# Kernel tuning notes

Measured on AMD Instinct MI355X. Metric: run time of the kernel, lower is better.

## Reference

```python
import jax, jax.numpy as jnp
import numpy as np

DIM = 768
HEADS = 12
DH = DIM // HEADS


def setup_inputs() -> dict:
    key = jax.random.key(0)
    ks = jax.random.split(key, 5)
    b, n = 2, 4096
    x = jax.random.normal(ks[0], (b, n, DIM), dtype=jnp.float32)
    # to_qkv: Linear(dim -> 3*heads*dh)
    w_qkv = jax.random.normal(ks[1], (DIM, 3 * HEADS * DH), dtype=jnp.float32) * (DIM ** -0.5)
    b_qkv = jax.random.normal(ks[2], (3 * HEADS * DH,), dtype=jnp.float32) * 0.01
    # out: Linear(heads*dh -> dim)
    w_out = jax.random.normal(ks[3], (HEADS * DH, DIM), dtype=jnp.float32) * ((HEADS * DH) ** -0.5)
    b_out = jax.random.normal(ks[4], (DIM,), dtype=jnp.float32) * 0.01
    return {"x": x, "w_qkv": w_qkv, "b_qkv": b_qkv, "w_out": w_out, "b_out": b_out}


def reference(x, w_qkv, b_qkv, w_out, b_out):
    b, n, _ = x.shape
    scale = DIM ** -0.5  # NOTE: module scales by dim**-0.5, not d_h**-0.5
    qkv = x @ w_qkv + b_qkv                        # [b, n, 3*h*d]
    q, k, v = jnp.split(qkv, 3, axis=-1)
    def to_heads(t):
        return t.reshape(b, n, HEADS, DH).transpose(0, 2, 1, 3)  # [b, h, n, d]
    q, k, v = to_heads(q), to_heads(k), to_heads(v)
    dots = jnp.einsum('bhid,bhjd->bhij', q, k) * scale  # [b, h, n, n]
    attn = jax.nn.softmax(dots, axis=-1)
    out = jnp.einsum('bhij,bhjd->bhid', attn, v)        # [b, h, n, d]
    out = out.transpose(0, 2, 1, 3).reshape(b, n, HEADS * DH)
    return out @ w_out + b_out
```

## Files before the change

kernel.cpp:

```cpp
#include <hip/hip_runtime.h>
#include <math.h>

#define DIM 768
#define HEADS 12
#define DH 64
#define NSEQ 4096
#define BATCH 2
#define BH (BATCH * HEADS)

typedef __attribute__((ext_vector_type(8))) short bf16x8;
typedef __attribute__((ext_vector_type(4))) float f32x4;

typedef const __attribute__((address_space(1))) unsigned char* as1_u8;
typedef __attribute__((address_space(3))) unsigned char* as3_u8;

__device__ __forceinline__ unsigned short f2bf(float x) {
  return (unsigned short)((__float_as_uint(x) + 0x8000u) >> 16);
}

__device__ __forceinline__ float exp2_fast(float x) {
  float r;
  asm volatile("v_exp_f32 %0, %1\n\ts_nop 0" : "=v"(r) : "v"(x));
  return r;
}

__device__ __forceinline__ void gl16(const void* g, void* l) {
  __builtin_amdgcn_global_load_lds((as1_u8)g, (as3_u8)l, 16, 0, 0);
}

__global__ __launch_bounds__(256) void transpose_cvt(const float* __restrict__ in,
                                                     unsigned short* __restrict__ out,
                                                     int K, int N) {
  __shared__ unsigned short s[32][34];
  int t = threadIdx.x;
  int tx = t & 31, ty = t >> 5;
  int n0 = blockIdx.x * 32, k0 = blockIdx.y * 32;
#pragma unroll
  for (int i = 0; i < 4; ++i) {
    int r = ty + i * 8;
    s[r][tx] = f2bf(in[(size_t)(k0 + r) * N + n0 + tx]);
  }
  __syncthreads();
#pragma unroll
  for (int i = 0; i < 4; ++i) {
    int r = ty + i * 8;
    out[(size_t)(n0 + r) * K + k0 + tx] = s[tx][r];
  }
}

__global__ __launch_bounds__(256) void vtrans(const unsigned short* __restrict__ Vb,
                                              unsigned short* __restrict__ Vt) {
  __shared__ unsigned short s[64][72];
  int t = threadIdx.x;
  int bh = blockIdx.y;
  int n0 = blockIdx.x * 64;
  const unsigned short* src = Vb + ((size_t)bh * NSEQ + n0) * DH;
#pragma unroll
  for (int i = 0; i < 2; ++i) {
    int idx = t + i * 256;
    int row = idx >> 3, ch = (idx & 7) * 8;
    *(uint4*)&s[row][ch] = *(const uint4*)(src + (size_t)row * DH + ch);
  }
  __syncthreads();
  unsigned short* dst = Vt + (size_t)bh * DH * NSEQ + n0;
#pragma unroll
  for (int i = 0; i < 2; ++i) {
    int idx = t + i * 256;
    int dh = idx >> 3, ch = (idx & 7) * 8;
    unsigned short tmp[8];
#pragma unroll
    for (int j = 0; j < 8; ++j) tmp[j] = s[ch + j][dh];
    *(uint4*)&dst[(size_t)dh * NSEQ + ch] = *(uint4*)tmp;
  }
}

template <int TM, int AF32>
__global__ __launch_bounds__(256, AF32 ? 3 : 4) void gemm_bt(
    const unsigned short* __restrict__ Ab, const float* __restrict__ Af,
    const unsigned short* __restrict__ Bt,
    const float* __restrict__ bias, float* __restrict__ outf,
    unsigned short* __restrict__ Qb, unsigned short* __restrict__ Kb,
    unsigned short* __restrict__ V0, int M, int N, int K, int mode) {
  constexpr int ABYTES = AF32 ? TM * 256 : TM * 128;
  __shared__ __align__(16) char Sraw[ABYTES + 128 * 128];
  float* As32 = (float*)Sraw;
  unsigned short* Asb = (unsigned short*)Sraw;
  unsigned short* Bs = (unsigned short*)(Sraw + ABYTES);
  constexpr int MI = TM / 32;
  const int t = threadIdx.x;
  const int wave = t >> 6, lane = t & 63;
  const int ln16 = lane & 15, quad = lane >> 4;
  const int sw = ln16 & 7;

  const int nbx = gridDim.x;
  const int nwg = nbx * gridDim.y;
  int bid = blockIdx.x + blockIdx.y * nbx;
  int nbid = (bid & 7) * (nwg >> 3) + (bid >> 3);
  const int cb = nbid % nbx, rb = nbid / nbx;

  const int rw = (wave >> 1) * (TM / 2);
  const int cw = (wave & 1) * 64;

  const int row8 = lane >> 3;
  const int csw = (lane & 7) ^ row8;
  const int r4 = lane >> 4;
  const int c16 = lane & 15;

  f32x4 acc[MI][4];
#pragma unroll
  for (int i = 0; i < MI; ++i)
#pragma unroll
    for (int j = 0; j < 4; ++j) acc[i][j] = (f32x4){0.f, 0.f, 0.f, 0.f};

  const unsigned short* gA =
      AF32 ? nullptr : (Ab + (size_t)(rb * TM + row8) * K + csw * 8);
  const unsigned short* gB = Bt + (size_t)(cb * 128 + row8) * K + csw * 8;

  for (int k0 = 0; k0 < K; k0 += 64) {
    __syncthreads();
    if (AF32) {
#pragma unroll
      for (int i = 0; i < TM / 16; ++i) {
        int rt = wave * (TM / 4) + i * 4 + r4;
        int csrc = c16 ^ (rt & 15);
        gl16(Af + (size_t)(rb * TM + rt) * K + k0 + csrc * 4,
             Sraw + (wave * (TM / 4) + i * 4) * 256);
      }
    } else {
#pragma unroll
      for (int i = 0; i < MI; ++i) {
        int rr = wave * (TM / 4) + i * 8;
        gl16(gA + (size_t)rr * K + k0, &Asb[rr * 64]);
      }
    }
#pragma unroll
    for (int i = 0; i < 4; ++i) {
      int rr = wave * 32 + i * 8;
      gl16(gB + (size_t)rr * K + k0, &Bs[rr * 64]);
    }
    asm volatile("s_waitcnt vmcnt(0)" ::: "memory");
    __syncthreads();

#pragma unroll
    for (int kh = 0; kh < 2; ++kh) {
      bf16x8 a[MI], b[4];
#pragma unroll
      for (int mi = 0; mi < MI; ++mi) {
        int row = rw + mi * 16 + ln16;
        if (AF32) {
          int cf0 = (kh * 8 + quad * 2) ^ ln16;
          int cf1 = (kh * 8 + quad * 2 + 1) ^ ln16;
          f32x4 lo = *(const f32x4*)(As32 + row * 64 + cf0 * 4);
          f32x4 hi = *(const f32x4*)(As32 + row * 64 + cf1 * 4);
          unsigned int u0, u1, u2, u3;
          asm("v_cvt_pk_bf16_f32 %0, %1, %2" : "=v"(u0) : "v"(lo[0]), "v"(lo[1]));
          asm("v_cvt_pk_bf16_f32 %0, %1, %2" : "=v"(u1) : "v"(lo[2]), "v"(lo[3]));
          asm("v_cvt_pk_bf16_f32 %0, %1, %2" : "=v"(u2) : "v"(hi[0]), "v"(hi[1]));
          asm("v_cvt_pk_bf16_f32 %0, %1, %2" : "=v"(u3) : "v"(hi[2]), "v"(hi[3]));
          union { unsigned int u[4]; bf16x8 v; } A8;
          A8.u[0] = u0; A8.u[1] = u1; A8.u[2] = u2; A8.u[3] = u3;
          a[mi] = A8.v;
        } else {
          a[mi] = *(const bf16x8*)&Asb[row * 64 + (((kh << 2) | quad) ^ sw) * 8];
        }
      }
#pragma unroll
      for (int ni = 0; ni < 4; ++ni) {
        int row = cw + ni * 16 + ln16;
        b[ni] = *(const bf16x8*)&Bs[row * 64 + (((kh << 2) | quad) ^ sw) * 8];
      }
#pragma unroll
      for (int mi = 0; mi < MI; ++mi)
#pragma unroll
        for (int ni = 0; ni < 4; ++ni)
          acc[mi][ni] = __builtin_amdgcn_mfma_f32_16x16x32_bf16(a[mi], b[ni],
                                                                acc[mi][ni], 0, 0, 0);
    }
  }

  if (mode == 0) {
    __syncthreads();
    const float scale = 0.0520587731f;
    int col0abs = cb * 128 + cw;
    int which = (col0abs >= 2 * DIM) ? 2 : ((col0abs >= DIM) ? 1 : 0);
    int h = (col0abs - which * DIM) >> 6;
    unsigned short* dstp = (which == 0) ? Qb : ((which == 1) ? Kb : V0);
    const float mul = (which == 0) ? scale : 1.f;
    float* Cs = (float*)Sraw + wave * (16 * 68);
    float bvv[4];
#pragma unroll
    for (int ni = 0; ni < 4; ++ni) bvv[ni] = bias[col0abs + ni * 16 + ln16];
#pragma unroll
    for (int mi = 0; mi < MI; ++mi) {
#pragma unroll
      for (int ni = 0; ni < 4; ++ni)
#pragma unroll
        for (int r = 0; r < 4; ++r)
          Cs[(quad * 4 + r) * 68 + ni * 16 + ln16] = (acc[mi][ni][r] + bvv[ni]) * mul;
      __asm__ volatile("s_waitcnt lgkmcnt(0)" ::: "memory");
      int token = rb * TM + rw + mi * 16 + ln16;
      int bb = token >> 12, nn = token & (NSEQ - 1);
      const float* src = &Cs[ln16 * 68 + quad * 16];
      float4 c0 = *(const float4*)(src + 0);
      float4 c1 = *(const float4*)(src + 4);
      float4 c2 = *(const float4*)(src + 8);
      float4 c3 = *(const float4*)(src + 12);
      unsigned short tmp[16];
      tmp[0] = f2bf(c0.x);  tmp[1] = f2bf(c0.y);  tmp[2] = f2bf(c0.z);  tmp[3] = f2bf(c0.w);
      tmp[4] = f2bf(c1.x);  tmp[5] = f2bf(c1.y);  tmp[6] = f2bf(c1.z);  tmp[7] = f2bf(c1.w);
      tmp[8] = f2bf(c2.x);  tmp[9] = f2bf(c2.y);  tmp[10] = f2bf(c2.z); tmp[11] = f2bf(c2.w);
      tmp[12] = f2bf(c3.x); tmp[13] = f2bf(c3.y); tmp[14] = f2bf(c3.z); tmp[15] = f2bf(c3.w);
      unsigned short* dp =
          dstp + ((size_t)(bb * HEADS + h) * NSEQ + nn) * DH + quad * 16;
      *(uint4*)&dp[0] = *(uint4*)&tmp[0];
      *(uint4*)&dp[8] = *(uint4*)&tmp[8];
      __asm__ volatile("s_waitcnt lgkmcnt(0)" ::: "memory");
    }
  } else {
#pragma unroll
    for (int ni = 0; ni < 4; ++ni) {
      int col = cb * 128 + cw + ni * 16 + ln16;
      float bv2 = bias[col];
#pragma unroll
      for (int mi = 0; mi < MI; ++mi)
#pragma unroll
        for (int r = 0; r < 4; ++r) {
          int token = rb * TM + rw + mi * 16 + quad * 4 + r;
          outf[(size_t)token * N + col] = acc[mi][ni][r] + bv2;
        }
    }
  }
}

__global__ __launch_bounds__(256, 3) void attn_mfma4(
    const unsigned short* __restrict__ Qg, const unsigned short* __restrict__ Kg,
    const unsigned short* __restrict__ Vtg, unsigned short* __restrict__ ctxb) {
  __shared__ unsigned short Ks[2][64][64];
  __shared__ unsigned short Vts[2][64][64];

  const int t = threadIdx.x;
  const int wave = t >> 6, lane = t & 63;
  const int ln16 = lane & 15, quad = lane >> 4;

  int bid = blockIdx.x + blockIdx.y * 32;
  int nbid = (bid & 7) * 96 + (bid >> 3);
  const int bh = nbid >> 5;
  const int q0 = (nbid & 31) * 128;

  const unsigned short* Qp = Qg + ((size_t)bh * NSEQ + q0 + wave * 32) * DH;
  bf16x8 qf[2][2];
#pragma unroll
  for (int mi = 0; mi < 2; ++mi)
#pragma unroll
    for (int kh = 0; kh < 2; ++kh)
      qf[mi][kh] = *(const bf16x8*)(Qp + (size_t)(mi * 16 + ln16) * DH + kh * 32 + quad * 8);

  f32x4 O[2][5];
#pragma unroll
  for (int mi = 0; mi < 2; ++mi)
#pragma unroll
    for (int nt = 0; nt < 5; ++nt) O[mi][nt] = (f32x4){0.f, 0.f, 0.f, 0.f};

  const unsigned short* Kbase = Kg + (size_t)bh * NSEQ * DH;
  const unsigned short* Vbase = Vtg + (size_t)bh * DH * NSEQ;

  const int row8 = lane >> 3;
  const int csw = (lane & 7) ^ row8;

  auto stage = [&](int b, int kk) {
#pragma unroll
    for (int i = 0; i < 2; ++i) {
      int rr = wave * 16 + i * 8;
      gl16(Kbase + (size_t)(kk + rr + row8) * DH + csw * 8, &Ks[b][rr][0]);
      gl16(Vbase + (size_t)(rr + row8) * NSEQ + kk + csw * 8, &Vts[b][rr][0]);
    }
  };

  union { unsigned int u[4]; bf16x8 v; } VO;
  {
    unsigned int ow = (ln16 == 0) ? 0x3F803F80u : 0u;
    VO.u[0] = ow; VO.u[1] = ow; VO.u[2] = ow; VO.u[3] = ow;
  }
  const bf16x8 vone = VO.v;

  stage(0, 0);
  const int sw = ln16 & 7;
  int buf = 0;

  for (int k0 = 0; k0 < NSEQ; k0 += 64) {
    asm volatile("s_waitcnt vmcnt(0)" ::: "memory");
    __syncthreads();
    if (k0 + 64 < NSEQ) stage(buf ^ 1, k0 + 64);

    f32x4 S[2][4];
    __builtin_amdgcn_s_setprio(1);
#pragma unroll
    for (int nt = 0; nt < 4; ++nt) {
      const unsigned short* kr = &Ks[buf][nt * 16 + ln16][0];
      bf16x8 kb0 = *(const bf16x8*)(kr + (quad ^ sw) * 8);
      bf16x8 kb1 = *(const bf16x8*)(kr + ((quad + 4) ^ sw) * 8);
#pragma unroll
      for (int mi = 0; mi < 2; ++mi) {
        f32x4 s = (f32x4){0.f, 0.f, 0.f, 0.f};
        s = __builtin_amdgcn_mfma_f32_16x16x32_bf16(kb0, qf[mi][0], s, 0, 0, 0);
        s = __builtin_amdgcn_mfma_f32_16x16x32_bf16(kb1, qf[mi][1], s, 0, 0, 0);
        S[mi][nt] = s;
      }
    }
    __builtin_amdgcn_s_setprio(0);

    bf16x8 pa[2][2];
#pragma unroll
    for (int mi = 0; mi < 2; ++mi) {
      unsigned int c[4][2];
#pragma unroll
      for (int nt = 0; nt < 4; ++nt) {
        float e0 = exp2_fast(S[mi][nt][0]);
        float e1 = exp2_fast(S[mi][nt][1]);
        float e2 = exp2_fast(S[mi][nt][2]);
        float e3 = exp2_fast(S[mi][nt][3]);
        asm volatile("v_cvt_pk_bf16_f32 %0, %1, %2" : "=v"(c[nt][0]) : "v"(e0), "v"(e1));
        asm volatile("v_cvt_pk_bf16_f32 %0, %1, %2" : "=v"(c[nt][1]) : "v"(e2), "v"(e3));
      }
#pragma unroll
      for (int kh = 0; kh < 2; ++kh) {
        unsigned int a0 = c[2 * kh][0], a1 = c[2 * kh][1];
        unsigned int a2 = c[2 * kh + 1][0], a3 = c[2 * kh + 1][1];
        asm volatile("v_permlane32_swap_b32 %0, %1" : "+v"(a0), "+v"(a2));
        asm volatile("v_permlane16_swap_b32 %0, %1" : "+v"(a0), "+v"(a2));
        asm volatile("v_permlane32_swap_b32 %0, %1" : "+v"(a1), "+v"(a3));
        asm volatile("v_permlane16_swap_b32 %0, %1" : "+v"(a1), "+v"(a3));
        union { unsigned int u[4]; bf16x8 v; } P;
        P.u[0] = a0; P.u[1] = a1; P.u[2] = a2; P.u[3] = a3;
        pa[mi][kh] = P.v;
      }
    }

    __builtin_amdgcn_s_setprio(1);
#pragma unroll
    for (int nt = 0; nt < 5; ++nt) {
      bf16x8 vb0, vb1;
      if (nt < 4) {
        const unsigned short* vr = &Vts[buf][nt * 16 + ln16][0];
        vb0 = *(const bf16x8*)(vr + (quad ^ sw) * 8);
        vb1 = *(const bf16x8*)(vr + ((quad + 4) ^ sw) * 8);
      } else {
        vb0 = vone; vb1 = vone;
      }
#pragma unroll
      for (int mi = 0; mi < 2; ++mi) {
        O[mi][nt] = __builtin_amdgcn_mfma_f32_16x16x32_bf16(pa[mi][0], vb0, O[mi][nt], 0, 0, 0);
        O[mi][nt] = __builtin_amdgcn_mfma_f32_16x16x32_bf16(pa[mi][1], vb1, O[mi][nt], 0, 0, 0);
      }
    }
    __builtin_amdgcn_s_setprio(0);
    buf ^= 1;
  }

  int bb = bh / HEADS, h = bh % HEADS;
#pragma unroll
  for (int mi = 0; mi < 2; ++mi)
#pragma unroll
    for (int r = 0; r < 4; ++r) {
      float lsum = O[mi][4][r];
      lsum = __shfl(lsum, lane & 48);
      float inv = 1.f / lsum;
      int token = q0 + wave * 32 + mi * 16 + quad * 4 + r;
      unsigned short* op = ctxb + ((size_t)(bb * NSEQ + token)) * DIM + h * DH;
#pragma unroll
      for (int nt = 0; nt < 4; ++nt)
        op[nt * 16 + ln16] = f2bf(O[mi][nt][r] * inv);
    }
}

extern "C" void kernel_launch(void* const* d_in, const int* in_sizes, int n_in,
                              void* d_out, int out_size, void* d_ws, size_t ws_size,
                              hipStream_t stream) {
  const float* x = (const float*)d_in[0];
  const float* w_qkv = (const float*)d_in[1];
  const float* b_qkv = (const float*)d_in[2];
  const float* w_out = (const float*)d_in[3];
  const float* b_out = (const float*)d_in[4];
  float* out = (float*)d_out;

  const size_t plane = (size_t)BH * NSEQ * DH;
  unsigned short* wqkvT = (unsigned short*)d_ws;
  unsigned short* woutT = wqkvT + (size_t)3 * DIM * DIM;
  unsigned short* Qb = woutT + (size_t)DIM * DIM;
  unsigned short* Kb = Qb + plane;
  unsigned short* V0 = Kb + plane;
  unsigned short* Vtb = V0 + plane;
  unsigned short* ctxb = Vtb + plane;

  transpose_cvt<<<dim3(3 * DIM / 32, DIM / 32), 256, 0, stream>>>(w_qkv, wqkvT, DIM, 3 * DIM);
  transpose_cvt<<<dim3(DIM / 32, DIM / 32), 256, 0, stream>>>(w_out, woutT, DIM, DIM);

  gemm_bt<128, 1><<<dim3(3 * DIM / 128, BATCH * NSEQ / 128), 256, 0, stream>>>(
      nullptr, x, wqkvT, b_qkv, nullptr, Qb, Kb, V0, BATCH * NSEQ, 3 * DIM, DIM, 0);

  vtrans<<<dim3(NSEQ / 64, BH), 256, 0, stream>>>(V0, Vtb);

  attn_mfma4<<<dim3(NSEQ / 128, BH), 256, 0, stream>>>(Qb, Kb, Vtb, ctxb);

  gemm_bt<64, 0><<<dim3(DIM / 128, BATCH * NSEQ / 64), 256, 0, stream>>>(
      ctxb, nullptr, woutT, b_out, out, nullptr, nullptr, nullptr, BATCH * NSEQ, DIM, DIM, 1);
}
```

Before: 256.8 us.

## Fuse V transpose into QKV GEMM epilogue and register-prefetch fp32 A

Removes the separate vtrans kernel by having the QKV GEMM epilogue write V directly in transposed [bh, dh, n] layout through an LDS staging tile. The fp32 A operand of the QKV GEMM is now prefetched into registers one k-step ahead and converted to bf16 before the LDS store, which halves A's LDS footprint and allows 4 blocks per CU. The output-projection epilogue is also staged through LDS to emit coalesced float4 stores. Tradeoffs are higher register pressure from the prefetch buffers and narrower per-lane transposed V stores.

```diff
diff --git a/kernel.cpp b/kernel.cpp
--- a/kernel.cpp
+++ b/kernel.cpp
@@ -48,42 +48,15 @@
   }
 }
 
-__global__ __launch_bounds__(256) void vtrans(const unsigned short* __restrict__ Vb,
-                                              unsigned short* __restrict__ Vt) {
-  __shared__ unsigned short s[64][72];
-  int t = threadIdx.x;
-  int bh = blockIdx.y;
-  int n0 = blockIdx.x * 64;
-  const unsigned short* src = Vb + ((size_t)bh * NSEQ + n0) * DH;
-#pragma unroll
-  for (int i = 0; i < 2; ++i) {
-    int idx = t + i * 256;
-    int row = idx >> 3, ch = (idx & 7) * 8;
-    *(uint4*)&s[row][ch] = *(const uint4*)(src + (size_t)row * DH + ch);
-  }
-  __syncthreads();
-  unsigned short* dst = Vt + (size_t)bh * DH * NSEQ + n0;
-#pragma unroll
-  for (int i = 0; i < 2; ++i) {
-    int idx = t + i * 256;
-    int dh = idx >> 3, ch = (idx & 7) * 8;
-    unsigned short tmp[8];
-#pragma unroll
-    for (int j = 0; j < 8; ++j) tmp[j] = s[ch + j][dh];
-    *(uint4*)&dst[(size_t)dh * NSEQ + ch] = *(uint4*)tmp;
-  }
-}
-
 template <int TM, int AF32>
-__global__ __launch_bounds__(256, AF32 ? 3 : 4) void gemm_bt(
+__global__ __launch_bounds__(256, 4) void gemm_bt(
     const unsigned short* __restrict__ Ab, const float* __restrict__ Af,
     const unsigned short* __restrict__ Bt,
     const float* __restrict__ bias, float* __restrict__ outf,
     unsigned short* __restrict__ Qb, unsigned short* __restrict__ Kb,
-    unsigned short* __restrict__ V0, int M, int N, int K, int mode) {
-  constexpr int ABYTES = AF32 ? TM * 256 : TM * 128;
+    unsigned short* __restrict__ Vt, int M, int N, int K, int mode) {
+  constexpr int ABYTES = TM * 128;
   __shared__ __align__(16) char Sraw[ABYTES + 128 * 128];
-  float* As32 = (float*)Sraw;
   unsigned short* Asb = (unsigned short*)Sraw;
   unsigned short* Bs = (unsigned short*)(Sraw + ABYTES);
   constexpr int MI = TM / 32;
@@ -103,8 +76,8 @@
 
   const int row8 = lane >> 3;
   const int csw = (lane & 7) ^ row8;
-  const int r4 = lane >> 4;
-  const int c16 = lane & 15;
+  const int r16 = lane >> 4;
+  const int c16l = lane & 15;
 
   f32x4 acc[MI][4];
 #pragma unroll
@@ -115,17 +88,35 @@
   const unsigned short* gA =
       AF32 ? nullptr : (Ab + (size_t)(rb * TM + row8) * K + csw * 8);
   const unsigned short* gB = Bt + (size_t)(cb * 128 + row8) * K + csw * 8;
+  const float* gAx =
+      AF32 ? (Af + (size_t)(rb * TM + wave * (TM / 4) + r16) * K + c16l * 4)
+           : nullptr;
+
+  float4 af[AF32 ? TM / 16 : 1];
+  auto loadA = [&](int k0) {
+#pragma unroll
+    for (int j = 0; j < TM / 16; ++j)
+      af[j] = *(const float4*)(gAx + (size_t)(j * 4) * K + k0);
+  };
+  auto writeA = [&]() {
+#pragma unroll
+    for (int j = 0; j < TM / 16; ++j) {
+      int row = wave * (TM / 4) + j * 4 + r16;
+      unsigned int u0, u1;
+      asm("v_cvt_pk_bf16_f32 %0, %1, %2" : "=v"(u0) : "v"(af[j].x), "v"(af[j].y));
+      asm("v_cvt_pk_bf16_f32 %0, %1, %2" : "=v"(u1) : "v"(af[j].z), "v"(af[j].w));
+      uint2 w; w.x = u0; w.y = u1;
+      int cs = (c16l >> 1) ^ (row & 7);
+      *(uint2*)&Asb[row * 64 + cs * 8 + (c16l & 1) * 4] = w;
+    }
+  };
+
+  if (AF32) loadA(0);
 
   for (int k0 = 0; k0 < K; k0 += 64) {
     __syncthreads();
     if (AF32) {
-#pragma unroll
-      for (int i = 0; i < TM / 16; ++i) {
-        int rt = wave * (TM / 4) + i * 4 + r4;
-        int csrc = c16 ^ (rt & 15);
-        gl16(Af + (size_t)(rb * TM + rt) * K + k0 + csrc * 4,
-             Sraw + (wave * (TM / 4) + i * 4) * 256);
-      }
+      writeA();
     } else {
 #pragma unroll
       for (int i = 0; i < MI; ++i) {
@@ -140,6 +131,7 @@
     }
     asm volatile("s_waitcnt vmcnt(0)" ::: "memory");
     __syncthreads();
+    if (AF32 && k0 + 64 < K) loadA(k0 + 64);
 
 #pragma unroll
     for (int kh = 0; kh < 2; ++kh) {
@@ -147,22 +139,7 @@
 #pragma unroll
       for (int mi = 0; mi < MI; ++mi) {
         int row = rw + mi * 16 + ln16;
-        if (AF32) {
-          int cf0 = (kh * 8 + quad * 2) ^ ln16;
-          int cf1 = (kh * 8 + quad * 2 + 1) ^ ln16;
-          f32x4 lo = *(const f32x4*)(As32 + row * 64 + cf0 * 4);
-          f32x4 hi = *(const f32x4*)(As32 + row * 64 + cf1 * 4);
-          unsigned int u0, u1, u2, u3;
-          asm("v_cvt_pk_bf16_f32 %0, %1, %2" : "=v"(u0) : "v"(lo[0]), "v"(lo[1]));
-          asm("v_cvt_pk_bf16_f32 %0, %1, %2" : "=v"(u1) : "v"(lo[2]), "v"(lo[3]));
-          asm("v_cvt_pk_bf16_f32 %0, %1, %2" : "=v"(u2) : "v"(hi[0]), "v"(hi[1]));
-          asm("v_cvt_pk_bf16_f32 %0, %1, %2" : "=v"(u3) : "v"(hi[2]), "v"(hi[3]));
-          union { unsigned int u[4]; bf16x8 v; } A8;
-          A8.u[0] = u0; A8.u[1] = u1; A8.u[2] = u2; A8.u[3] = u3;
-          a[mi] = A8.v;
-        } else {
-          a[mi] = *(const bf16x8*)&Asb[row * 64 + (((kh << 2) | quad) ^ sw) * 8];
-        }
+        a[mi] = *(const bf16x8*)&Asb[row * 64 + (((kh << 2) | quad) ^ sw) * 8];
       }
 #pragma unroll
       for (int ni = 0; ni < 4; ++ni) {
@@ -184,50 +161,87 @@
     int col0abs = cb * 128 + cw;
     int which = (col0abs >= 2 * DIM) ? 2 : ((col0abs >= DIM) ? 1 : 0);
     int h = (col0abs - which * DIM) >> 6;
-    unsigned short* dstp = (which == 0) ? Qb : ((which == 1) ? Kb : V0);
     const float mul = (which == 0) ? scale : 1.f;
     float* Cs = (float*)Sraw + wave * (16 * 68);
     float bvv[4];
 #pragma unroll
     for (int ni = 0; ni < 4; ++ni) bvv[ni] = bias[col0abs + ni * 16 + ln16];
+    int bb = (rb * TM) >> 12;
+
+    if (which == 2) {
+#pragma unroll
+      for (int mi = 0; mi < MI; ++mi) {
+#pragma unroll
+        for (int ni = 0; ni < 4; ++ni)
+#pragma unroll
+          for (int r = 0; r < 4; ++r)
+            Cs[(quad * 4 + r) * 68 + ni * 16 + ln16] = acc[mi][ni][r] + bvv[ni];
+        __asm__ volatile("s_waitcnt lgkmcnt(0)" ::: "memory");
+        int n0 = (rb * TM + rw + mi * 16) & (NSEQ - 1);
+        unsigned short tmp[16];
+#pragma unroll
+        for (int r = 0; r < 16; ++r) tmp[r] = f2bf(Cs[r * 68 + lane]);
+        unsigned short* dp =
+            Vt + ((size_t)((bb * HEADS + h) * DH + lane)) * NSEQ + n0;
+        *(uint4*)&dp[0] = *(uint4*)&tmp[0];
+        *(uint4*)&dp[8] = *(uint4*)&tmp[8];
+        __asm__ volatile("s_waitcnt lgkmcnt(0)" ::: "memory");
+      }
+    } else {
+      unsigned short* dstp = (which == 0) ? Qb : Kb;
+#pragma unroll
+      for (int mi = 0; mi < MI; ++mi) {
+#pragma unroll
+        for (int ni = 0; ni < 4; ++ni)
+#pragma unroll
+          for (int r = 0; r < 4; ++r)
+            Cs[(quad * 4 + r) * 68 + ni * 16 + ln16] = (acc[mi][ni][r] + bvv[ni]) * mul;
+        __asm__ volatile("s_waitcnt lgkmcnt(0)" ::: "memory");
+        int token = rb * TM + rw + mi * 16 + ln16;
+        int nn = token & (NSEQ - 1);
+        const float* src = &Cs[ln16 * 68 + quad * 16];
+        float4 c0 = *(const float4*)(src + 0);
+        float4 c1 = *(const float4*)(src + 4);
+        float4 c2 = *(const float4*)(src + 8);
+        float4 c3 = *(const float4*)(src + 12);
+        unsigned short tmp[16];
+        tmp[0] = f2bf(c0.x);  tmp[1] = f2bf(c0.y);  tmp[2] = f2bf(c0.z);  tmp[3] = f2bf(c0.w);
+        tmp[4] = f2bf(c1.x);  tmp[5] = f2bf(c1.y);  tmp[6] = f2bf(c1.z);  tmp[7] = f2bf(c1.w);
+        tmp[8] = f2bf(c2.x);  tmp[9] = f2bf(c2.y);  tmp[10] = f2bf(c2.z); tmp[11] = f2bf(c2.w);
+        tmp[12] = f2bf(c3.x); tmp[13] = f2bf(c3.y); tmp[14] = f2bf(c3.z); tmp[15] = f2bf(c3.w);
+        unsigned short* dp =
+            dstp + ((size_t)(bb * HEADS + h) * NSEQ + nn) * DH + quad * 16;
+        *(uint4*)&dp[0] = *(uint4*)&tmp[0];
+        *(uint4*)&dp[8] = *(uint4*)&tmp[8];
+        __asm__ volatile("s_waitcnt lgkmcnt(0)" ::: "memory");
+      }
+    }
+  } else {
+    __syncthreads();
+    float* Cs = (float*)Sraw + wave * (16 * 68);
+    float bvv[4];
+#pragma unroll
+    for (int ni = 0; ni < 4; ++ni) bvv[ni] = bias[cb * 128 + cw + ni * 16 + ln16];
 #pragma unroll
     for (int mi = 0; mi < MI; ++mi) {
 #pragma unroll
       for (int ni = 0; ni < 4; ++ni)
 #pragma unroll
         for (int r = 0; r < 4; ++r)
-          Cs[(quad * 4 + r) * 68 + ni * 16 + ln16] = (acc[mi][ni][r] + bvv[ni]) * mul;
+          Cs[(quad * 4 + r) * 68 + ni * 16 + ln16] = acc[mi][ni][r] + bvv[ni];
       __asm__ volatile("s_waitcnt lgkmcnt(0)" ::: "memory");
       int token = rb * TM + rw + mi * 16 + ln16;
-      int bb = token >> 12, nn = token & (NSEQ - 1);
       const float* src = &Cs[ln16 * 68 + quad * 16];
       float4 c0 = *(const float4*)(src + 0);
       float4 c1 = *(const float4*)(src + 4);
       float4 c2 = *(const float4*)(src + 8);
       float4 c3 = *(const float4*)(src + 12);
-      unsigned short tmp[16];
-      tmp[0] = f2bf(c0.x);  tmp[1] = f2bf(c0.y);  tmp[2] = f2bf(c0.z);  tmp[3] = f2bf(c0.w);
-      tmp[4] = f2bf(c1.x);  tmp[5] = f2bf(c1.y);  tmp[6] = f2bf(c1.z);  tmp[7] = f2bf(c1.w);
-      tmp[8] = f2bf(c2.x);  tmp[9] = f2bf(c2.y);  tmp[10] = f2bf(c2.z); tmp[11] = f2bf(c2.w);
-      tmp[12] = f2bf(c3.x); tmp[13] = f2bf(c3.y); tmp[14] = f2bf(c3.z); tmp[15] = f2bf(c3.w);
-      unsigned short* dp =
-          dstp + ((size_t)(bb * HEADS + h) * NSEQ + nn) * DH + quad * 16;
-      *(uint4*)&dp[0] = *(uint4*)&tmp[0];
-      *(uint4*)&dp[8] = *(uint4*)&tmp[8];
+      float* op = outf + (size_t)token * N + cb * 128 + cw + quad * 16;
+      *(float4*)(op + 0) = c0;
+      *(float4*)(op + 4) = c1;
+      *(float4*)(op + 8) = c2;
+      *(float4*)(op + 12) = c3;
       __asm__ volatile("s_waitcnt lgkmcnt(0)" ::: "memory");
-    }
-  } else {
-#pragma unroll
-    for (int ni = 0; ni < 4; ++ni) {
-      int col = cb * 128 + cw + ni * 16 + ln16;
-      float bv2 = bias[col];
-#pragma unroll
-      for (int mi = 0; mi < MI; ++mi)
-#pragma unroll
-        for (int r = 0; r < 4; ++r) {
-          int token = rb * TM + rw + mi * 16 + quad * 4 + r;
-          outf[(size_t)token * N + col] = acc[mi][ni][r] + bv2;
-        }
     }
   }
 }
@@ -388,17 +402,14 @@
   unsigned short* woutT = wqkvT + (size_t)3 * DIM * DIM;
   unsigned short* Qb = woutT + (size_t)DIM * DIM;
   unsigned short* Kb = Qb + plane;
-  unsigned short* V0 = Kb + plane;
-  unsigned short* Vtb = V0 + plane;
+  unsigned short* Vtb = Kb + plane;
   unsigned short* ctxb = Vtb + plane;
 
   transpose_cvt<<<dim3(3 * DIM / 32, DIM / 32), 256, 0, stream>>>(w_qkv, wqkvT, DIM, 3 * DIM);
   transpose_cvt<<<dim3(DIM / 32, DIM / 32), 256, 0, stream>>>(w_out, woutT, DIM, DIM);
 
   gemm_bt<128, 1><<<dim3(3 * DIM / 128, BATCH * NSEQ / 128), 256, 0, stream>>>(
-      nullptr, x, wqkvT, b_qkv, nullptr, Qb, Kb, V0, BATCH * NSEQ, 3 * DIM, DIM, 0);
-
-  vtrans<<<dim3(NSEQ / 64, BH), 256, 0, stream>>>(V0, Vtb);
+      nullptr, x, wqkvT, b_qkv, nullptr, Qb, Kb, Vtb, BATCH * NSEQ, 3 * DIM, DIM, 0);
 
   attn_mfma4<<<dim3(NSEQ / 128, BH), 256, 0, stream>>>(Qb, Kb, Vtb, ctxb);
 
```

Result: slower. 459.7 us (+79.0%).
